# Kernel tuning notes

Hardware: AMD Instinct MI355X
Metric: run time of the kernel (lower is better)

## Reference

```python
import jax, jax.numpy as jnp
import numpy as np

DIM = 768
HEADS = 16
HEAD_DIM = DIM // HEADS  # 48


def setup_inputs() -> dict:
    key = jax.random.key(0)
    ks = jax.random.split(key, 9)
    s = 1.0 / np.sqrt(DIM)
    inp = {
        "x": jax.random.normal(ks[0], (4, 2048, DIM), dtype=jnp.float32),
        "Wq": jax.random.uniform(ks[1], (DIM, DIM), jnp.float32, -s, s),
        "bq": jax.random.uniform(ks[2], (DIM,), jnp.float32, -s, s),
        "Wk": jax.random.uniform(ks[3], (DIM, DIM), jnp.float32, -s, s),
        "bk": jax.random.uniform(ks[4], (DIM,), jnp.float32, -s, s),
        "Wv": jax.random.uniform(ks[5], (DIM, DIM), jnp.float32, -s, s),
        "bv": jax.random.uniform(ks[6], (DIM,), jnp.float32, -s, s),
        "Wo": jax.random.uniform(ks[7], (DIM, DIM), jnp.float32, -s, s),
        "bo": jax.random.uniform(ks[8], (DIM,), jnp.float32, -s, s),
    }
    return inp


def reference(x, Wq, bq, Wk, bk, Wv, bv, Wo, bo):
    B, S, _ = x.shape
    # torch nn.Linear: y = x @ W.T + b
    q = x @ Wq.T + bq
    k = x @ Wk.T + bk
    v = x @ Wv.T + bv
    # split heads: (B, H, S, Dh)
    q = q.reshape(B, S, HEADS, HEAD_DIM).transpose(0, 2, 1, 3)
    k = k.reshape(B, S, HEADS, HEAD_DIM).transpose(0, 2, 1, 3)
    v = v.reshape(B, S, HEADS, HEAD_DIM).transpose(0, 2, 1, 3)
    score = jnp.einsum("bhqd,bhkd->bhqk", q, k) / jnp.sqrt(jnp.float32(HEAD_DIM))
    attn = jax.nn.softmax(score, axis=-1)
    out = jnp.einsum("bhqk,bhkd->bhqd", attn, v)
    out = out.transpose(0, 2, 1, 3).reshape(B, S, DIM)
    return out @ Wo.T + bo
```

## Files before the change

### kernel.cpp

```cpp
#include <hip/hip_runtime.h>

#define DIM 768
#define SEQ 2048
#define NB 4
#define NH 16
#define DH 48
#define DP 64
#define BHN (NB*NH)
#define MTOK (NB*SEQ)

typedef __attribute__((ext_vector_type(8))) short bf16x8;
typedef __attribute__((ext_vector_type(4))) float f32x4;
typedef __attribute__((ext_vector_type(4))) unsigned int u32x4;

__device__ __forceinline__ unsigned short f32_to_bf16(float f) {
    union { float f; unsigned int u; } v; v.f = f;
    unsigned int r = v.u + 0x7fff + ((v.u >> 16) & 1);
    return (unsigned short)(r >> 16);
}

#if __has_builtin(__builtin_amdgcn_exp2f)
#define EXP2F(x) __builtin_amdgcn_exp2f(x)
#else
#define EXP2F(x) exp2f(x)
#endif

#define GL_LDS16(g, l) __builtin_amdgcn_global_load_lds( \
    (const __attribute__((address_space(1))) void*)(g),  \
    (__attribute__((address_space(3))) void*)(l), 16, 0, 0)

__global__ void cvt_f32_bf16(const float* __restrict__ src, unsigned short* __restrict__ dst, int n) {
    int i = (blockIdx.x * blockDim.x + threadIdx.x) * 4;
    if (i + 3 < n) {
        const float4 v = *(const float4*)(src + i);
        ushort4 o;
        o.x = f32_to_bf16(v.x); o.y = f32_to_bf16(v.y);
        o.z = f32_to_bf16(v.z); o.w = f32_to_bf16(v.w);
        *(ushort4*)(dst + i) = o;
    }
}

__global__ void cvt4_f32_bf16(const float* __restrict__ a, const float* __restrict__ b,
                              const float* __restrict__ c, const float* __restrict__ d,
                              unsigned short* __restrict__ dst, int n_each) {
    const float* srcs[4] = {a, b, c, d};
    const float* src = srcs[blockIdx.y];
    unsigned short* out = dst + blockIdx.y * n_each;
    int i = (blockIdx.x * blockDim.x + threadIdx.x) * 4;
    if (i + 3 < n_each) {
        const float4 v = *(const float4*)(src + i);
        ushort4 o;
        o.x = f32_to_bf16(v.x); o.y = f32_to_bf16(v.y);
        o.z = f32_to_bf16(v.z); o.w = f32_to_bf16(v.w);
        *(ushort4*)(out + i) = o;
    }
}

#define BK 32

__global__ __launch_bounds__(256) void qkv_gemm(
    const unsigned short* __restrict__ xb,
    const unsigned short* __restrict__ wb,
    const float* __restrict__ bq, const float* __restrict__ bk, const float* __restrict__ bv,
    unsigned short* __restrict__ Qb, unsigned short* __restrict__ Kb, unsigned short* __restrict__ Vt)
{
    const int z = blockIdx.z;
    const unsigned short* W = wb + z * (DIM * DIM);
    const float* bias = (z == 0) ? bq : (z == 1) ? bk : bv;
    const int row0 = blockIdx.x * 128;
    const int col0 = blockIdx.y * 128;

    __shared__ __align__(16) short As[128 * BK];
    __shared__ __align__(16) short Bs[128 * BK];

    const int tid = threadIdx.x;
    const int lane = tid & 63;
    const int w = tid >> 6;
    const int wy = w >> 1, wx = w & 1;
    const int l15 = lane & 15, quad = lane >> 4;
    const int lr = lane >> 2;
    const int lco = (lane & 3) * 8;

    f32x4 acc[4][4];
    for (int mi = 0; mi < 4; ++mi) for (int ni = 0; ni < 4; ++ni)
        for (int r = 0; r < 4; ++r) acc[mi][ni][r] = 0.f;

    for (int kt = 0; kt < DIM / BK; ++kt) {
        #pragma unroll
        for (int j = 0; j < 2; ++j) {
            const int c = w * 2 + j;
            GL_LDS16(&xb[(row0 + c * 16 + lr) * DIM + kt * BK + lco], &As[c * 512]);
            GL_LDS16(&W [(col0 + c * 16 + lr) * DIM + kt * BK + lco], &Bs[c * 512]);
        }
        __syncthreads();
        bf16x8 af[4], bfr[4];
        #pragma unroll
        for (int mi = 0; mi < 4; ++mi)
            af[mi] = *(const bf16x8*)&As[(wy * 64 + mi * 16 + l15) * BK + quad * 8];
        #pragma unroll
        for (int ni = 0; ni < 4; ++ni)
            bfr[ni] = *(const bf16x8*)&Bs[(wx * 64 + ni * 16 + l15) * BK + quad * 8];
        #pragma unroll
        for (int mi = 0; mi < 4; ++mi)
            #pragma unroll
            for (int ni = 0; ni < 4; ++ni)
                acc[mi][ni] = __builtin_amdgcn_mfma_f32_16x16x32_bf16(af[mi], bfr[ni], acc[mi][ni], 0, 0, 0);
        __syncthreads();
    }

    const float qscale = 0.14433756729740643f * 1.4426950408889634f;

    if (z == 2) {
        #pragma unroll
        for (int mi = 0; mi < 4; ++mi) {
            #pragma unroll
            for (int ni = 0; ni < 4; ++ni) {
                int col = col0 + wx * 64 + ni * 16 + l15;
                int h = col / DH, d = col - h * DH;
                int row = row0 + wy * 64 + mi * 16 + quad * 4;
                int b = row >> 11, s = row & 2047;
                float bi = bias[col];
                union { ushort4 v; unsigned short e[4]; } pk;
                #pragma unroll
                for (int r = 0; r < 4; ++r)
                    pk.e[r] = f32_to_bf16(acc[mi][ni][r] + bi);
                *(ushort4*)&Vt[((b * NH + h) * DP + d) * SEQ + s] = pk.v;
            }
        }
    } else {
        #pragma unroll
        for (int mi = 0; mi < 4; ++mi) {
            #pragma unroll
            for (int ni = 0; ni < 4; ++ni) {
                #pragma unroll
                for (int r = 0; r < 4; ++r) {
                    int row = row0 + wy * 64 + mi * 16 + quad * 4 + r;
                    int col = col0 + wx * 64 + ni * 16 + l15;
                    float v = acc[mi][ni][r] + bias[col];
                    int b = row >> 11, s = row & 2047;
                    int h = col / DH, d = col - h * DH;
                    int bh = b * NH + h;
                    if (z == 0) Qb[(bh * SEQ + s) * DP + d] = f32_to_bf16(v * qscale);
                    else        Kb[(bh * SEQ + s) * DP + d] = f32_to_bf16(v);
                }
            }
        }
    }
}

__global__ __launch_bounds__(256) void out_gemm(
    const unsigned short* __restrict__ ab,
    const unsigned short* __restrict__ Wo,
    const float* __restrict__ bo,
    float* __restrict__ out)
{
    const int row0 = blockIdx.x * 128;
    const int col0 = blockIdx.y * 128;

    __shared__ __align__(16) short As[128 * BK];
    __shared__ __align__(16) short Bs[128 * BK];

    const int tid = threadIdx.x;
    const int lane = tid & 63;
    const int w = tid >> 6;
    const int wy = w >> 1, wx = w & 1;
    const int l15 = lane & 15, quad = lane >> 4;
    const int lr = lane >> 2;
    const int lco = (lane & 3) * 8;

    f32x4 acc[4][4];
    for (int mi = 0; mi < 4; ++mi) for (int ni = 0; ni < 4; ++ni)
        for (int r = 0; r < 4; ++r) acc[mi][ni][r] = 0.f;

    for (int kt = 0; kt < DIM / BK; ++kt) {
        #pragma unroll
        for (int j = 0; j < 2; ++j) {
            const int c = w * 2 + j;
            GL_LDS16(&ab[(row0 + c * 16 + lr) * DIM + kt * BK + lco], &As[c * 512]);
            GL_LDS16(&Wo[(col0 + c * 16 + lr) * DIM + kt * BK + lco], &Bs[c * 512]);
        }
        __syncthreads();
        bf16x8 af[4], bfr[4];
        #pragma unroll
        for (int mi = 0; mi < 4; ++mi)
            af[mi] = *(const bf16x8*)&As[(wy * 64 + mi * 16 + l15) * BK + quad * 8];
        #pragma unroll
        for (int ni = 0; ni < 4; ++ni)
            bfr[ni] = *(const bf16x8*)&Bs[(wx * 64 + ni * 16 + l15) * BK + quad * 8];
        #pragma unroll
        for (int mi = 0; mi < 4; ++mi)
            #pragma unroll
            for (int ni = 0; ni < 4; ++ni)
                acc[mi][ni] = __builtin_amdgcn_mfma_f32_16x16x32_bf16(af[mi], bfr[ni], acc[mi][ni], 0, 0, 0);
        __syncthreads();
    }

    #pragma unroll
    for (int mi = 0; mi < 4; ++mi)
        #pragma unroll
        for (int ni = 0; ni < 4; ++ni)
            #pragma unroll
            for (int r = 0; r < 4; ++r) {
                int row = row0 + wy * 64 + mi * 16 + quad * 4 + r;
                int col = col0 + wx * 64 + ni * 16 + l15;
                out[row * DIM + col] = acc[mi][ni][r] + bo[col];
            }
}

__device__ __forceinline__ int keyperm(int a) {
    return (a & 32) + ((a & 12) << 1) + ((a & 16) >> 2) + (a & 3);
}

__global__ __launch_bounds__(512, 4) void attn_kernel(
    const unsigned short* __restrict__ Qb,
    const unsigned short* __restrict__ Kb,
    const unsigned short* __restrict__ Vt,
    unsigned short* __restrict__ Ob)
{
    const int bh = blockIdx.y;
    const int tile = blockIdx.x;
    const int tid = threadIdx.x;
    const int w = tid >> 6;
    const int lane = tid & 63;
    const int l15 = lane & 15, quad = lane >> 4;

    const unsigned short* Qh = Qb + bh * SEQ * DP;
    const unsigned short* Kh = Kb + bh * SEQ * DP;
    const unsigned short* Vh = Vt + bh * DP * SEQ;
    const int q0 = tile * 256 + w * 32;

    __shared__ __align__(16) short Ks[64 * 64];
    __shared__ __align__(16) short Vs[48 * 64];

    bf16x8 aq[2][2];
    #pragma unroll
    for (int m = 0; m < 2; ++m)
        #pragma unroll
        for (int ks = 0; ks < 2; ++ks)
            aq[m][ks] = *(const bf16x8*)&Qh[(q0 + m * 16 + l15) * DP + ks * 32 + quad * 8];
    if (quad >= 2) {
        const bf16x8 z8 = {0, 0, 0, 0, 0, 0, 0, 0};
        aq[0][1] = z8;
        aq[1][1] = z8;
    }

    f32x4 o[2][3];
    #pragma unroll
    for (int m = 0; m < 2; ++m) for (int ni = 0; ni < 3; ++ni)
        for (int r = 0; r < 4; ++r) o[m][ni][r] = 0.f;
    float ls[2][4];
    #pragma unroll
    for (int m = 0; m < 2; ++m) for (int r = 0; r < 4; ++r) ls[m][r] = 0.f;

    const f32x4 FZ = {0.f, 0.f, 0.f, 0.f};

    const int sa = tid >> 3;
    const int sc_ = tid & 7;
    const int lc8 = (sc_ ^ (sa & 7)) * 8;
    const int ka = keyperm(sa);
    const int lds_w = sa * 64 + sc_ * 8;
    const bool vld = (sa < 48);

    bf16x8 kr, vr;
    kr = *(const bf16x8*)&Kh[ka * DP + lc8];
    if (vld) vr = *(const bf16x8*)&Vh[sa * SEQ + lc8];

    for (int kt = 0; kt < SEQ / 64; ++kt) {
        __syncthreads();
        *(bf16x8*)&Ks[lds_w] = kr;
        if (vld) *(bf16x8*)&Vs[lds_w] = vr;
        if (kt + 1 < SEQ / 64) {
            const int k0n = (kt + 1) * 64;
            kr = *(const bf16x8*)&Kh[(k0n + ka) * DP + lc8];
            if (vld) vr = *(const bf16x8*)&Vh[sa * SEQ + k0n + lc8];
        }
        __syncthreads();

        bf16x8 ak0[4], ak1[4];
        #pragma unroll
        for (int n = 0; n < 4; ++n) {
            ak0[n] = *(const bf16x8*)&Ks[(n * 16 + l15) * 64 + ((quad ^ (l15 & 7)) * 8)];
            ak1[n] = *(const bf16x8*)&Ks[(n * 16 + l15) * 64 + (((4 + quad) ^ (l15 & 7)) * 8)];
        }
        f32x4 sc[2][4];
        #pragma unroll
        for (int n = 0; n < 4; ++n) {
            sc[0][n] = __builtin_amdgcn_mfma_f32_16x16x32_bf16(ak0[n], aq[0][0], FZ, 0, 0, 0);
            sc[1][n] = __builtin_amdgcn_mfma_f32_16x16x32_bf16(ak0[n], aq[1][0], FZ, 0, 0, 0);
        }
        #pragma unroll
        for (int n = 0; n < 4; ++n) {
            sc[0][n] = __builtin_amdgcn_mfma_f32_16x16x32_bf16(ak1[n], aq[0][1], sc[0][n], 0, 0, 0);
            sc[1][n] = __builtin_amdgcn_mfma_f32_16x16x32_bf16(ak1[n], aq[1][1], sc[1][n], 0, 0, 0);
        }

        bf16x8 av[2][3];
        #pragma unroll
        for (int ks = 0; ks < 2; ++ks)
            #pragma unroll
            for (int mt = 0; mt < 3; ++mt)
                av[ks][mt] = *(const bf16x8*)&Vs[(mt * 16 + l15) * 64 + (((ks * 4 + quad) ^ (l15 & 7)) * 8)];

        #pragma unroll
        for (int m = 0; m < 2; ++m) {
            union { u32x4 u; bf16x8 h; } bp[2];
            #pragma unroll
            for (int ks = 0; ks < 2; ++ks) {
                #pragma unroll
                for (int w2 = 0; w2 < 4; ++w2) {
                    const int j0 = 2 * w2, j1 = 2 * w2 + 1;
                    float p0 = EXP2F(sc[m][2 * ks + (j0 >> 2)][j0 & 3]);
                    float p1 = EXP2F(sc[m][2 * ks + (j1 >> 2)][j1 & 3]);
                    ls[m][w2] += (p0 + p1);
                    bp[ks].u[w2] = __builtin_amdgcn_perm(__float_as_uint(p1), __float_as_uint(p0), 0x07060302u);
                }
            }
            #pragma unroll
            for (int ks = 0; ks < 2; ++ks)
                #pragma unroll
                for (int mt = 0; mt < 3; ++mt)
                    o[m][mt] = __builtin_amdgcn_mfma_f32_16x16x32_bf16(av[ks][mt], bp[ks].h, o[m][mt], 0, 0, 0);
        }
    }

    const int b = bh >> 4, h = bh & 15;
    #pragma unroll
    for (int m = 0; m < 2; ++m) {
        float lsum = (ls[m][0] + ls[m][1]) + (ls[m][2] + ls[m][3]);
        lsum += __shfl_xor(lsum, 16);
        lsum += __shfl_xor(lsum, 32);
        float inv = 1.f / lsum;
        #pragma unroll
        for (int mt = 0; mt < 3; ++mt)
            #pragma unroll
            for (int r = 0; r < 4; ++r) {
                int token = b * SEQ + q0 + m * 16 + l15;
                int d = mt * 16 + quad * 4 + r;
                Ob[token * DIM + h * DH + d] = f32_to_bf16(o[m][mt][r] * inv);
            }
    }
}

extern "C" void kernel_launch(void* const* d_in, const int* in_sizes, int n_in,
                              void* d_out, int out_size, void* d_ws, size_t ws_size,
                              hipStream_t stream) {
    const float* x  = (const float*)d_in[0];
    const float* Wq = (const float*)d_in[1]; const float* bq = (const float*)d_in[2];
    const float* Wk = (const float*)d_in[3]; const float* bk = (const float*)d_in[4];
    const float* Wv = (const float*)d_in[5]; const float* bv = (const float*)d_in[6];
    const float* Wo = (const float*)d_in[7]; const float* bo = (const float*)d_in[8];

    unsigned char* ws = (unsigned char*)d_ws;
    unsigned short* xb = (unsigned short*)(ws);
    unsigned short* wb = (unsigned short*)(ws + 12582912);
    unsigned short* Qb = (unsigned short*)(ws + 17301504);
    unsigned short* Kb = (unsigned short*)(ws + 34078720);
    unsigned short* Vt = (unsigned short*)(ws + 50855936);
    unsigned short* Ob = (unsigned short*)(ws + 67633152);

    cvt_f32_bf16<<<6144, 256, 0, stream>>>(x, xb, MTOK * DIM);
    cvt4_f32_bf16<<<dim3(576, 4), 256, 0, stream>>>(Wq, Wk, Wv, Wo, wb, DIM * DIM);

    qkv_gemm<<<dim3(MTOK / 128, DIM / 128, 3), 256, 0, stream>>>(xb, wb, bq, bk, bv, Qb, Kb, Vt);
    attn_kernel<<<dim3(SEQ / 256, BHN), 512, 0, stream>>>(Qb, Kb, Vt, Ob);
    out_gemm<<<dim3(MTOK / 128, DIM / 128), 256, 0, stream>>>(Ob, wb + 3 * DIM * DIM, bo, (float*)d_out);
}
```

Measured before the change: 220.8 us.

## Deepen GEMM K-tile to 64 with XOR-swizzled LDS and reorder attention grid

```diff
diff --git a/kernel.cpp b/kernel.cpp
--- a/kernel.cpp
+++ b/kernel.cpp
@@ -56,7 +56,7 @@
     }
 }
 
-#define BK 32
+#define BKG 64
 
 __global__ __launch_bounds__(256) void qkv_gemm(
     const unsigned short* __restrict__ xb,
@@ -70,41 +70,44 @@
     const int row0 = blockIdx.x * 128;
     const int col0 = blockIdx.y * 128;
 
-    __shared__ __align__(16) short As[128 * BK];
-    __shared__ __align__(16) short Bs[128 * BK];
+    __shared__ __align__(16) short As[128 * BKG];
+    __shared__ __align__(16) short Bs[128 * BKG];
 
     const int tid = threadIdx.x;
     const int lane = tid & 63;
     const int w = tid >> 6;
     const int wy = w >> 1, wx = w & 1;
     const int l15 = lane & 15, quad = lane >> 4;
-    const int lr = lane >> 2;
-    const int lco = (lane & 3) * 8;
+    const int srow = lane >> 3;
+    const int scol = ((lane & 7) ^ srow) * 8;
 
     f32x4 acc[4][4];
     for (int mi = 0; mi < 4; ++mi) for (int ni = 0; ni < 4; ++ni)
         for (int r = 0; r < 4; ++r) acc[mi][ni][r] = 0.f;
 
-    for (int kt = 0; kt < DIM / BK; ++kt) {
-        #pragma unroll
-        for (int j = 0; j < 2; ++j) {
-            const int c = w * 2 + j;
-            GL_LDS16(&xb[(row0 + c * 16 + lr) * DIM + kt * BK + lco], &As[c * 512]);
-            GL_LDS16(&W [(col0 + c * 16 + lr) * DIM + kt * BK + lco], &Bs[c * 512]);
-        }
-        __syncthreads();
-        bf16x8 af[4], bfr[4];
-        #pragma unroll
-        for (int mi = 0; mi < 4; ++mi)
-            af[mi] = *(const bf16x8*)&As[(wy * 64 + mi * 16 + l15) * BK + quad * 8];
-        #pragma unroll
-        for (int ni = 0; ni < 4; ++ni)
-            bfr[ni] = *(const bf16x8*)&Bs[(wx * 64 + ni * 16 + l15) * BK + quad * 8];
-        #pragma unroll
-        for (int mi = 0; mi < 4; ++mi)
+    for (int kt = 0; kt < DIM / BKG; ++kt) {
+        #pragma unroll
+        for (int j = 0; j < 4; ++j) {
+            const int c = w * 4 + j;
+            GL_LDS16(&xb[(row0 + c * 8 + srow) * DIM + kt * BKG + scol], &As[c * 512]);
+            GL_LDS16(&W [(col0 + c * 8 + srow) * DIM + kt * BKG + scol], &Bs[c * 512]);
+        }
+        __syncthreads();
+        #pragma unroll
+        for (int ks = 0; ks < 2; ++ks) {
+            bf16x8 af[4], bfr[4];
+            #pragma unroll
+            for (int mi = 0; mi < 4; ++mi)
+                af[mi] = *(const bf16x8*)&As[(wy * 64 + mi * 16 + l15) * BKG + (((ks * 4 + quad) ^ (l15 & 7)) * 8)];
             #pragma unroll
             for (int ni = 0; ni < 4; ++ni)
-                acc[mi][ni] = __builtin_amdgcn_mfma_f32_16x16x32_bf16(af[mi], bfr[ni], acc[mi][ni], 0, 0, 0);
+                bfr[ni] = *(const bf16x8*)&Bs[(wx * 64 + ni * 16 + l15) * BKG + (((ks * 4 + quad) ^ (l15 & 7)) * 8)];
+            #pragma unroll
+            for (int mi = 0; mi < 4; ++mi)
+                #pragma unroll
+                for (int ni = 0; ni < 4; ++ni)
+                    acc[mi][ni] = __builtin_amdgcn_mfma_f32_16x16x32_bf16(af[mi], bfr[ni], acc[mi][ni], 0, 0, 0);
+        }
         __syncthreads();
     }
 
@@ -157,41 +160,44 @@
     const int row0 = blockIdx.x * 128;
     const int col0 = blockIdx.y * 128;
 
-    __shared__ __align__(16) short As[128 * BK];
-    __shared__ __align__(16) short Bs[128 * BK];
+    __shared__ __align__(16) short As[128 * BKG];
+    __shared__ __align__(16) short Bs[128 * BKG];
 
     const int tid = threadIdx.x;
     const int lane = tid & 63;
     const int w = tid >> 6;
     const int wy = w >> 1, wx = w & 1;
     const int l15 = lane & 15, quad = lane >> 4;
-    const int lr = lane >> 2;
-    const int lco = (lane & 3) * 8;
+    const int srow = lane >> 3;
+    const int scol = ((lane & 7) ^ srow) * 8;
 
     f32x4 acc[4][4];
     for (int mi = 0; mi < 4; ++mi) for (int ni = 0; ni < 4; ++ni)
         for (int r = 0; r < 4; ++r) acc[mi][ni][r] = 0.f;
 
-    for (int kt = 0; kt < DIM / BK; ++kt) {
-        #pragma unroll
-        for (int j = 0; j < 2; ++j) {
-            const int c = w * 2 + j;
-            GL_LDS16(&ab[(row0 + c * 16 + lr) * DIM + kt * BK + lco], &As[c * 512]);
-            GL_LDS16(&Wo[(col0 + c * 16 + lr) * DIM + kt * BK + lco], &Bs[c * 512]);
-        }
-        __syncthreads();
-        bf16x8 af[4], bfr[4];
-        #pragma unroll
-        for (int mi = 0; mi < 4; ++mi)
-            af[mi] = *(const bf16x8*)&As[(wy * 64 + mi * 16 + l15) * BK + quad * 8];
-        #pragma unroll
-        for (int ni = 0; ni < 4; ++ni)
-            bfr[ni] = *(const bf16x8*)&Bs[(wx * 64 + ni * 16 + l15) * BK + quad * 8];
-        #pragma unroll
-        for (int mi = 0; mi < 4; ++mi)
+    for (int kt = 0; kt < DIM / BKG; ++kt) {
+        #pragma unroll
+        for (int j = 0; j < 4; ++j) {
+            const int c = w * 4 + j;
+            GL_LDS16(&ab[(row0 + c * 8 + srow) * DIM + kt * BKG + scol], &As[c * 512]);
+            GL_LDS16(&Wo[(col0 + c * 8 + srow) * DIM + kt * BKG + scol], &Bs[c * 512]);
+        }
+        __syncthreads();
+        #pragma unroll
+        for (int ks = 0; ks < 2; ++ks) {
+            bf16x8 af[4], bfr[4];
+            #pragma unroll
+            for (int mi = 0; mi < 4; ++mi)
+                af[mi] = *(const bf16x8*)&As[(wy * 64 + mi * 16 + l15) * BKG + (((ks * 4 + quad) ^ (l15 & 7)) * 8)];
             #pragma unroll
             for (int ni = 0; ni < 4; ++ni)
-                acc[mi][ni] = __builtin_amdgcn_mfma_f32_16x16x32_bf16(af[mi], bfr[ni], acc[mi][ni], 0, 0, 0);
+                bfr[ni] = *(const bf16x8*)&Bs[(wx * 64 + ni * 16 + l15) * BKG + (((ks * 4 + quad) ^ (l15 & 7)) * 8)];
+            #pragma unroll
+            for (int mi = 0; mi < 4; ++mi)
+                #pragma unroll
+                for (int ni = 0; ni < 4; ++ni)
+                    acc[mi][ni] = __builtin_amdgcn_mfma_f32_16x16x32_bf16(af[mi], bfr[ni], acc[mi][ni], 0, 0, 0);
+        }
         __syncthreads();
     }
 
@@ -217,8 +223,8 @@
     const unsigned short* __restrict__ Vt,
     unsigned short* __restrict__ Ob)
 {
-    const int bh = blockIdx.y;
-    const int tile = blockIdx.x;
+    const int bh = blockIdx.x;
+    const int tile = blockIdx.y;
     const int tid = threadIdx.x;
     const int w = tid >> 6;
     const int lane = tid & 63;
@@ -362,6 +368,6 @@
     cvt4_f32_bf16<<<dim3(576, 4), 256, 0, stream>>>(Wq, Wk, Wv, Wo, wb, DIM * DIM);
 
     qkv_gemm<<<dim3(MTOK / 128, DIM / 128, 3), 256, 0, stream>>>(xb, wb, bq, bk, bv, Qb, Kb, Vt);
-    attn_kernel<<<dim3(SEQ / 256, BHN), 512, 0, stream>>>(Qb, Kb, Vt, Ob);
+    attn_kernel<<<dim3(BHN, SEQ / 256), 512, 0, stream>>>(Qb, Kb, Vt, Ob);
     out_gemm<<<dim3(MTOK / 128, DIM / 128), 256, 0, stream>>>(Ob, wb + 3 * DIM * DIM, bo, (float*)d_out);
 }
```

After: 227.2 us. 1.03x slower.

## Enlarge QKV GEMM tile to 256 rows, swizzle LDS, reorder attention grid

Applied to the files above, without the earlier changes.

```diff
diff --git a/kernel.cpp b/kernel.cpp
--- a/kernel.cpp
+++ b/kernel.cpp
@@ -58,7 +58,7 @@
 
 #define BK 32
 
-__global__ __launch_bounds__(256) void qkv_gemm(
+__global__ __launch_bounds__(512, 4) void qkv_gemm(
     const unsigned short* __restrict__ xb,
     const unsigned short* __restrict__ wb,
     const float* __restrict__ bq, const float* __restrict__ bk, const float* __restrict__ bv,
@@ -67,10 +67,10 @@
     const int z = blockIdx.z;
     const unsigned short* W = wb + z * (DIM * DIM);
     const float* bias = (z == 0) ? bq : (z == 1) ? bk : bv;
-    const int row0 = blockIdx.x * 128;
+    const int row0 = blockIdx.x * 256;
     const int col0 = blockIdx.y * 128;
 
-    __shared__ __align__(16) short As[128 * BK];
+    __shared__ __align__(16) short As[256 * BK];
     __shared__ __align__(16) short Bs[128 * BK];
 
     const int tid = threadIdx.x;
@@ -79,7 +79,7 @@
     const int wy = w >> 1, wx = w & 1;
     const int l15 = lane & 15, quad = lane >> 4;
     const int lr = lane >> 2;
-    const int lco = (lane & 3) * 8;
+    const int scol = (((lane & 3) ^ (lr & 3)) * 8);
 
     f32x4 acc[4][4];
     for (int mi = 0; mi < 4; ++mi) for (int ni = 0; ni < 4; ++ni)
@@ -87,19 +87,23 @@
 
     for (int kt = 0; kt < DIM / BK; ++kt) {
         #pragma unroll
-        for (int j = 0; j < 2; ++j) {
-            const int c = w * 2 + j;
-            GL_LDS16(&xb[(row0 + c * 16 + lr) * DIM + kt * BK + lco], &As[c * 512]);
-            GL_LDS16(&W [(col0 + c * 16 + lr) * DIM + kt * BK + lco], &Bs[c * 512]);
+        for (int j = 0; j < 3; ++j) {
+            const int c = w * 3 + j;
+            if (c < 16) {
+                GL_LDS16(&xb[(row0 + c * 16 + lr) * DIM + kt * BK + scol], &As[c * 512]);
+            } else {
+                const int cb = c - 16;
+                GL_LDS16(&W[(col0 + cb * 16 + lr) * DIM + kt * BK + scol], &Bs[cb * 512]);
+            }
         }
         __syncthreads();
         bf16x8 af[4], bfr[4];
         #pragma unroll
         for (int mi = 0; mi < 4; ++mi)
-            af[mi] = *(const bf16x8*)&As[(wy * 64 + mi * 16 + l15) * BK + quad * 8];
+            af[mi] = *(const bf16x8*)&As[(wy * 64 + mi * 16 + l15) * BK + ((quad ^ (l15 & 3)) * 8)];
         #pragma unroll
         for (int ni = 0; ni < 4; ++ni)
-            bfr[ni] = *(const bf16x8*)&Bs[(wx * 64 + ni * 16 + l15) * BK + quad * 8];
+            bfr[ni] = *(const bf16x8*)&Bs[(wx * 64 + ni * 16 + l15) * BK + ((quad ^ (l15 & 3)) * 8)];
         #pragma unroll
         for (int mi = 0; mi < 4; ++mi)
             #pragma unroll
@@ -166,7 +170,7 @@
     const int wy = w >> 1, wx = w & 1;
     const int l15 = lane & 15, quad = lane >> 4;
     const int lr = lane >> 2;
-    const int lco = (lane & 3) * 8;
+    const int scol = (((lane & 3) ^ (lr & 3)) * 8);
 
     f32x4 acc[4][4];
     for (int mi = 0; mi < 4; ++mi) for (int ni = 0; ni < 4; ++ni)
@@ -176,17 +180,17 @@
         #pragma unroll
         for (int j = 0; j < 2; ++j) {
             const int c = w * 2 + j;
-            GL_LDS16(&ab[(row0 + c * 16 + lr) * DIM + kt * BK + lco], &As[c * 512]);
-            GL_LDS16(&Wo[(col0 + c * 16 + lr) * DIM + kt * BK + lco], &Bs[c * 512]);
+            GL_LDS16(&ab[(row0 + c * 16 + lr) * DIM + kt * BK + scol], &As[c * 512]);
+            GL_LDS16(&Wo[(col0 + c * 16 + lr) * DIM + kt * BK + scol], &Bs[c * 512]);
         }
         __syncthreads();
         bf16x8 af[4], bfr[4];
         #pragma unroll
         for (int mi = 0; mi < 4; ++mi)
-            af[mi] = *(const bf16x8*)&As[(wy * 64 + mi * 16 + l15) * BK + quad * 8];
+            af[mi] = *(const bf16x8*)&As[(wy * 64 + mi * 16 + l15) * BK + ((quad ^ (l15 & 3)) * 8)];
         #pragma unroll
         for (int ni = 0; ni < 4; ++ni)
-            bfr[ni] = *(const bf16x8*)&Bs[(wx * 64 + ni * 16 + l15) * BK + quad * 8];
+            bfr[ni] = *(const bf16x8*)&Bs[(wx * 64 + ni * 16 + l15) * BK + ((quad ^ (l15 & 3)) * 8)];
         #pragma unroll
         for (int mi = 0; mi < 4; ++mi)
             #pragma unroll
@@ -217,8 +221,8 @@
     const unsigned short* __restrict__ Vt,
     unsigned short* __restrict__ Ob)
 {
-    const int bh = blockIdx.y;
-    const int tile = blockIdx.x;
+    const int bh = blockIdx.x;
+    const int tile = blockIdx.y;
     const int tid = threadIdx.x;
     const int w = tid >> 6;
     const int lane = tid & 63;
@@ -361,7 +365,7 @@
     cvt_f32_bf16<<<6144, 256, 0, stream>>>(x, xb, MTOK * DIM);
     cvt4_f32_bf16<<<dim3(576, 4), 256, 0, stream>>>(Wq, Wk, Wv, Wo, wb, DIM * DIM);
 
-    qkv_gemm<<<dim3(MTOK / 128, DIM / 128, 3), 256, 0, stream>>>(xb, wb, bq, bk, bv, Qb, Kb, Vt);
-    attn_kernel<<<dim3(SEQ / 256, BHN), 512, 0, stream>>>(Qb, Kb, Vt, Ob);
+    qkv_gemm<<<dim3(MTOK / 256, DIM / 128, 3), 512, 0, stream>>>(xb, wb, bq, bk, bv, Qb, Kb, Vt);
+    attn_kernel<<<dim3(BHN, SEQ / 256), 512, 0, stream>>>(Qb, Kb, Vt, Ob);
     out_gemm<<<dim3(MTOK / 128, DIM / 128), 256, 0, stream>>>(Ob, wb + 3 * DIM * DIM, bo, (float*)d_out);
 }
```

Measured after the change: 234.0 us. 1.06x slower.

## Give each attention wave 64 query rows with 256-thread blocks

Applied to the files above, without the earlier changes.

```diff
diff --git a/kernel.cpp b/kernel.cpp
--- a/kernel.cpp
+++ b/kernel.cpp
@@ -211,14 +211,14 @@
     return (a & 32) + ((a & 12) << 1) + ((a & 16) >> 2) + (a & 3);
 }
 
-__global__ __launch_bounds__(512, 4) void attn_kernel(
+__global__ __launch_bounds__(256, 2) void attn_kernel(
     const unsigned short* __restrict__ Qb,
     const unsigned short* __restrict__ Kb,
     const unsigned short* __restrict__ Vt,
     unsigned short* __restrict__ Ob)
 {
-    const int bh = blockIdx.y;
-    const int tile = blockIdx.x;
+    const int bh = blockIdx.x;
+    const int tile = blockIdx.y;
     const int tid = threadIdx.x;
     const int w = tid >> 6;
     const int lane = tid & 63;
@@ -227,52 +227,66 @@
     const unsigned short* Qh = Qb + bh * SEQ * DP;
     const unsigned short* Kh = Kb + bh * SEQ * DP;
     const unsigned short* Vh = Vt + bh * DP * SEQ;
-    const int q0 = tile * 256 + w * 32;
+    const int q0 = tile * 256 + w * 64;
 
     __shared__ __align__(16) short Ks[64 * 64];
     __shared__ __align__(16) short Vs[48 * 64];
 
-    bf16x8 aq[2][2];
-    #pragma unroll
-    for (int m = 0; m < 2; ++m)
+    bf16x8 aq[4][2];
+    #pragma unroll
+    for (int m = 0; m < 4; ++m)
         #pragma unroll
         for (int ks = 0; ks < 2; ++ks)
             aq[m][ks] = *(const bf16x8*)&Qh[(q0 + m * 16 + l15) * DP + ks * 32 + quad * 8];
     if (quad >= 2) {
         const bf16x8 z8 = {0, 0, 0, 0, 0, 0, 0, 0};
-        aq[0][1] = z8;
-        aq[1][1] = z8;
-    }
-
-    f32x4 o[2][3];
-    #pragma unroll
-    for (int m = 0; m < 2; ++m) for (int ni = 0; ni < 3; ++ni)
+        #pragma unroll
+        for (int m = 0; m < 4; ++m) aq[m][1] = z8;
+    }
+
+    f32x4 o[4][3];
+    #pragma unroll
+    for (int m = 0; m < 4; ++m) for (int ni = 0; ni < 3; ++ni)
         for (int r = 0; r < 4; ++r) o[m][ni][r] = 0.f;
-    float ls[2][4];
-    #pragma unroll
-    for (int m = 0; m < 2; ++m) for (int r = 0; r < 4; ++r) ls[m][r] = 0.f;
+    float ls[4][2];
+    #pragma unroll
+    for (int m = 0; m < 4; ++m) { ls[m][0] = 0.f; ls[m][1] = 0.f; }
 
     const f32x4 FZ = {0.f, 0.f, 0.f, 0.f};
 
-    const int sa = tid >> 3;
-    const int sc_ = tid & 7;
-    const int lc8 = (sc_ ^ (sa & 7)) * 8;
-    const int ka = keyperm(sa);
-    const int lds_w = sa * 64 + sc_ * 8;
-    const bool vld = (sa < 48);
-
-    bf16x8 kr, vr;
-    kr = *(const bf16x8*)&Kh[ka * DP + lc8];
-    if (vld) vr = *(const bf16x8*)&Vh[sa * SEQ + lc8];
+    const int ra = tid >> 2;
+    const int pc = tid & 3;
+    const int lcA = ((pc ^ (ra & 7)) * 8);
+    const int lcB = (((pc + 4) ^ (ra & 7)) * 8);
+    const int kaR = keyperm(ra);
+    const int ldsA = ra * 64 + pc * 8;
+    const int ldsB = ra * 64 + (pc + 4) * 8;
+    const bool vld = (tid < 192);
+
+    bf16x8 kr0, kr1, vr0, vr1;
+    kr0 = *(const bf16x8*)&Kh[kaR * DP + lcA];
+    kr1 = *(const bf16x8*)&Kh[kaR * DP + lcB];
+    if (vld) {
+        vr0 = *(const bf16x8*)&Vh[ra * SEQ + lcA];
+        vr1 = *(const bf16x8*)&Vh[ra * SEQ + lcB];
+    }
 
     for (int kt = 0; kt < SEQ / 64; ++kt) {
         __syncthreads();
-        *(bf16x8*)&Ks[lds_w] = kr;
-        if (vld) *(bf16x8*)&Vs[lds_w] = vr;
+        *(bf16x8*)&Ks[ldsA] = kr0;
+        *(bf16x8*)&Ks[ldsB] = kr1;
+        if (vld) {
+            *(bf16x8*)&Vs[ldsA] = vr0;
+            *(bf16x8*)&Vs[ldsB] = vr1;
+        }
         if (kt + 1 < SEQ / 64) {
             const int k0n = (kt + 1) * 64;
-            kr = *(const bf16x8*)&Kh[(k0n + ka) * DP + lc8];
-            if (vld) vr = *(const bf16x8*)&Vh[sa * SEQ + k0n + lc8];
+            kr0 = *(const bf16x8*)&Kh[(k0n + kaR) * DP + lcA];
+            kr1 = *(const bf16x8*)&Kh[(k0n + kaR) * DP + lcB];
+            if (vld) {
+                vr0 = *(const bf16x8*)&Vh[ra * SEQ + k0n + lcA];
+                vr1 = *(const bf16x8*)&Vh[ra * SEQ + k0n + lcB];
+            }
         }
         __syncthreads();
 
@@ -282,18 +296,6 @@
             ak0[n] = *(const bf16x8*)&Ks[(n * 16 + l15) * 64 + ((quad ^ (l15 & 7)) * 8)];
             ak1[n] = *(const bf16x8*)&Ks[(n * 16 + l15) * 64 + (((4 + quad) ^ (l15 & 7)) * 8)];
         }
-        f32x4 sc[2][4];
-        #pragma unroll
-        for (int n = 0; n < 4; ++n) {
-            sc[0][n] = __builtin_amdgcn_mfma_f32_16x16x32_bf16(ak0[n], aq[0][0], FZ, 0, 0, 0);
-            sc[1][n] = __builtin_amdgcn_mfma_f32_16x16x32_bf16(ak0[n], aq[1][0], FZ, 0, 0, 0);
-        }
-        #pragma unroll
-        for (int n = 0; n < 4; ++n) {
-            sc[0][n] = __builtin_amdgcn_mfma_f32_16x16x32_bf16(ak1[n], aq[0][1], sc[0][n], 0, 0, 0);
-            sc[1][n] = __builtin_amdgcn_mfma_f32_16x16x32_bf16(ak1[n], aq[1][1], sc[1][n], 0, 0, 0);
-        }
-
         bf16x8 av[2][3];
         #pragma unroll
         for (int ks = 0; ks < 2; ++ks)
@@ -302,31 +304,48 @@
                 av[ks][mt] = *(const bf16x8*)&Vs[(mt * 16 + l15) * 64 + (((ks * 4 + quad) ^ (l15 & 7)) * 8)];
 
         #pragma unroll
-        for (int m = 0; m < 2; ++m) {
-            union { u32x4 u; bf16x8 h; } bp[2];
-            #pragma unroll
-            for (int ks = 0; ks < 2; ++ks) {
+        for (int mp = 0; mp < 2; ++mp) {
+            const int m0 = 2 * mp, m1 = 2 * mp + 1;
+            f32x4 sc[2][4];
+            #pragma unroll
+            for (int n = 0; n < 4; ++n) {
+                sc[0][n] = __builtin_amdgcn_mfma_f32_16x16x32_bf16(ak0[n], aq[m0][0], FZ, 0, 0, 0);
+                sc[1][n] = __builtin_amdgcn_mfma_f32_16x16x32_bf16(ak0[n], aq[m1][0], FZ, 0, 0, 0);
+            }
+            #pragma unroll
+            for (int n = 0; n < 4; ++n) {
+                sc[0][n] = __builtin_amdgcn_mfma_f32_16x16x32_bf16(ak1[n], aq[m0][1], sc[0][n], 0, 0, 0);
+                sc[1][n] = __builtin_amdgcn_mfma_f32_16x16x32_bf16(ak1[n], aq[m1][1], sc[1][n], 0, 0, 0);
+            }
+            union { u32x4 u; bf16x8 h; } bp[2][2];
+            #pragma unroll
+            for (int mi = 0; mi < 2; ++mi) {
                 #pragma unroll
-                for (int w2 = 0; w2 < 4; ++w2) {
-                    const int j0 = 2 * w2, j1 = 2 * w2 + 1;
-                    float p0 = EXP2F(sc[m][2 * ks + (j0 >> 2)][j0 & 3]);
-                    float p1 = EXP2F(sc[m][2 * ks + (j1 >> 2)][j1 & 3]);
-                    ls[m][w2] += (p0 + p1);
-                    bp[ks].u[w2] = __builtin_amdgcn_perm(__float_as_uint(p1), __float_as_uint(p0), 0x07060302u);
+                for (int ks = 0; ks < 2; ++ks) {
+                    #pragma unroll
+                    for (int w2 = 0; w2 < 4; ++w2) {
+                        const int j0 = 2 * w2, j1 = 2 * w2 + 1;
+                        float p0 = EXP2F(sc[mi][2 * ks + (j0 >> 2)][j0 & 3]);
+                        float p1 = EXP2F(sc[mi][2 * ks + (j1 >> 2)][j1 & 3]);
+                        ls[2 * mp + mi][w2 & 1] += (p0 + p1);
+                        bp[mi][ks].u[w2] = __builtin_amdgcn_perm(__float_as_uint(p1), __float_as_uint(p0), 0x07060302u);
+                    }
                 }
             }
             #pragma unroll
             for (int ks = 0; ks < 2; ++ks)
                 #pragma unroll
-                for (int mt = 0; mt < 3; ++mt)
-                    o[m][mt] = __builtin_amdgcn_mfma_f32_16x16x32_bf16(av[ks][mt], bp[ks].h, o[m][mt], 0, 0, 0);
+                for (int mt = 0; mt < 3; ++mt) {
+                    o[m0][mt] = __builtin_amdgcn_mfma_f32_16x16x32_bf16(av[ks][mt], bp[0][ks].h, o[m0][mt], 0, 0, 0);
+                    o[m1][mt] = __builtin_amdgcn_mfma_f32_16x16x32_bf16(av[ks][mt], bp[1][ks].h, o[m1][mt], 0, 0, 0);
+                }
         }
     }
 
     const int b = bh >> 4, h = bh & 15;
     #pragma unroll
-    for (int m = 0; m < 2; ++m) {
-        float lsum = (ls[m][0] + ls[m][1]) + (ls[m][2] + ls[m][3]);
+    for (int m = 0; m < 4; ++m) {
+        float lsum = ls[m][0] + ls[m][1];
         lsum += __shfl_xor(lsum, 16);
         lsum += __shfl_xor(lsum, 32);
         float inv = 1.f / lsum;
@@ -362,6 +381,6 @@
     cvt4_f32_bf16<<<dim3(576, 4), 256, 0, stream>>>(Wq, Wk, Wv, Wo, wb, DIM * DIM);
 
     qkv_gemm<<<dim3(MTOK / 128, DIM / 128, 3), 256, 0, stream>>>(xb, wb, bq, bk, bv, Qb, Kb, Vt);
-    attn_kernel<<<dim3(SEQ / 256, BHN), 512, 0, stream>>>(Qb, Kb, Vt, Ob);
+    attn_kernel<<<dim3(BHN, SEQ / 256), 256, 0, stream>>>(Qb, Kb, Vt, Ob);
     out_gemm<<<dim3(MTOK / 128, DIM / 128), 256, 0, stream>>>(Ob, wb + 3 * DIM * DIM, bo, (float*)d_out);
 }
```

Measured after the change: 218.2 us. Within noise of the previous version (-1.2%).
